# Optimization experiments

Measured on AMD Instinct MI355X. Metric: run time of the kernel, lower is better.

## Reference

```python
import jax, jax.numpy as jnp
import numpy as np

T, B, IN, HID, OUT = 100, 2048, 784, 100, 10
BETA = 0.9      # snn.Leaky(beta=0.9)
THRESH = 1.0    # snntorch default threshold
ALPHA = 2.0     # snntorch default ATan surrogate alpha

@jax.custom_vjp
def fire(x):
    # Heaviside spike with ATan surrogate gradient (snntorch default).
    return (x > 0).astype(x.dtype)

def _fire_fwd(x):
    return fire(x), x

def _fire_bwd(x, g):
    return (g * (ALPHA / 2) / (1 + (jnp.pi / 2 * ALPHA * x) ** 2),)

fire.defvjp(_fire_fwd, _fire_bwd)

def setup_inputs() -> dict:
    key = jax.random.key(0)
    k1, k2, k3 = jax.random.split(key, 3)
    x_seq = jax.random.normal(k1, (T, B, IN), dtype=jnp.float32)
    # nn.Linear weights are [out_features, in_features], bias=False
    w1 = jax.random.normal(k2, (HID, IN), dtype=jnp.float32) * (1.0 / np.sqrt(IN))
    w2 = jax.random.normal(k3, (OUT, HID), dtype=jnp.float32) * (1.0 / np.sqrt(HID))
    return {"x_seq": x_seq, "w1": w1, "w2": w2}

def _leaky_step(mem, cur):
    # snntorch Leaky, reset_mechanism='subtract':
    # reset = H(mem_prev - thresh) (detached); mem = beta*mem + input - reset*thresh; spk = fire(mem - thresh)
    reset = jax.lax.stop_gradient((mem > THRESH).astype(mem.dtype))
    mem = BETA * mem + cur - reset * THRESH
    spk = fire(mem - THRESH)
    return spk, mem

def reference(x_seq, w1, w2):
    batch = x_seq.shape[1]
    def step(carry, x_t):
        mem1, mem2 = carry
        spk1, mem1 = _leaky_step(mem1, x_t @ w1.T)      # [B,HID]
        spk2, mem2 = _leaky_step(mem2, spk1 @ w2.T)     # [B,OUT]
        return (mem1, mem2), spk2
    init = (jnp.zeros((batch, HID), x_seq.dtype),
            jnp.zeros((batch, OUT), x_seq.dtype))
    _, spk2_seq = jax.lax.scan(step, init, x_seq)
    return spk2_seq.sum(axis=0)  # spk2_sum: [B, OUT]
```

## Files before the change

kernel.cpp:

```cpp
#include <hip/hip_runtime.h>

#define T_STEPS 100
#define B_SZ    2048
#define IN_DIM  784
#define HID_DIM 100
#define OUT_DIM 10
#define BN      112
#define BMR     64
#define KC      16
#define NSTEP   (IN_DIM / KC)
#define XLP     84
#define WLP     112

typedef double f64x4 __attribute__((ext_vector_type(4)));
#define MFMA64(a, b, c) __builtin_amdgcn_mfma_f64_16x16x4f64((a), (b), (c), 0, 0, 0)

__global__ void pad_w1(const float* __restrict__ w1, float* __restrict__ w1p) {
  int i = blockIdx.x * 256 + threadIdx.x;
  if (i < BN * IN_DIM) w1p[i] = (i < HID_DIM * IN_DIM) ? w1[i] : 0.0f;
}

__global__ __launch_bounds__(256, 4)
void snn_gemm1(const float* __restrict__ x,
               const float* __restrict__ w1p,
               double* __restrict__ cur)
{
  const int tid  = threadIdx.x;
  const int lane = tid & 63;
  const int wv   = tid >> 6;
  const int kg   = lane >> 4;
  const int il   = lane & 15;
  const long rowBase = (long)blockIdx.x * BMR;

  __shared__ float xls[2][KC][XLP];
  __shared__ float wls[2][KC][WLP];

  const int xrow = tid >> 2;
  const int xq   = (tid & 3) * 4;
  const float* xsrc = x + (rowBase + xrow) * (long)IN_DIM + xq;
  const int  wrow = tid >> 1;
  const int  skh  = (tid & 1) * 8;
  const float* wsrc = w1p + (long)wrow * IN_DIM + skh;
  const bool   dow  = tid < 2 * BN;

  float4 xg, wa, wb;
  auto LOAD = [&](int s) {
    xg = *reinterpret_cast<const float4*>(xsrc + s * KC);
    if (dow) {
      const float4* wp = reinterpret_cast<const float4*>(wsrc + s * KC);
      wa = wp[0]; wb = wp[1];
    }
  };
  auto STORE = [&](int buf) {
    xls[buf][xq + 0][xrow] = xg.x; xls[buf][xq + 1][xrow] = xg.y;
    xls[buf][xq + 2][xrow] = xg.z; xls[buf][xq + 3][xrow] = xg.w;
    if (dow) {
      wls[buf][skh + 0][wrow] = wa.x; wls[buf][skh + 1][wrow] = wa.y;
      wls[buf][skh + 2][wrow] = wa.z; wls[buf][skh + 3][wrow] = wa.w;
      wls[buf][skh + 4][wrow] = wb.x; wls[buf][skh + 5][wrow] = wb.y;
      wls[buf][skh + 6][wrow] = wb.z; wls[buf][skh + 7][wrow] = wb.w;
    }
  };

  LOAD(0);

  f64x4 z = {0.0, 0.0, 0.0, 0.0};
  const double eil = (double)il;
  const double d0 = (kg == 0) ? 1.0 : 0.0;
  const double d1 = (kg == 1) ? 1.0 : 0.0;
  const double d2 = (kg == 2) ? 1.0 : 0.0;
  const double d3 = (kg == 3) ? 1.0 : 0.0;
  const f64x4 Prow0 = MFMA64(eil, d0, z);
  const f64x4 Prow1 = MFMA64(eil, d1, z);
  const f64x4 Pcol0 = MFMA64(d0, eil, z);
  const f64x4 Pcol1 = MFMA64(d1, eil, z);
  const f64x4 Pv0   = MFMA64(d0, d0, z);
  const f64x4 Pv1   = MFMA64(d1, d1, z);
  const f64x4 Pv2   = MFMA64(d2, d2, z);
  const f64x4 Pv3   = MFMA64(d3, d3, z);

  bool okl = true;
  int rowof[4], colof[4];
#pragma unroll
  for (int r = 0; r < 4; ++r) {
    okl = okl && (Pv0[r] == 1.0) && (Pv1[r] == 1.0) && (Pv2[r] == 1.0) && (Pv3[r] == 1.0);
    okl = okl && (Prow0[r] == Prow1[r]) && (Pcol0[r] == Pcol1[r]);
    const int rr = (int)Prow0[r];
    const int cc = (int)Pcol0[r];
    okl = okl && ((double)rr == Prow0[r]) && (rr >= 0) && (rr < 16);
    okl = okl && ((double)cc == Pcol0[r]) && (cc >= 0) && (cc < 16);
    rowof[r] = rr; colof[r] = cc;
  }
  if (__all(okl ? 1 : 0) == 0) {
#pragma unroll
    for (int r = 0; r < 4; ++r) { rowof[r] = kg * 4 + r; colof[r] = il; }
  }

  f64x4 acc[7];
#pragma unroll
  for (int ht = 0; ht < 7; ++ht) acc[ht] = z;

  STORE(0); LOAD(1);
  __syncthreads();

#pragma unroll 1
  for (int s = 0; s < NSTEP; ++s) {
    if (s + 1 < NSTEP) STORE((s + 1) & 1);
    if (s + 2 < NSTEP) LOAD(s + 2);
    const int buf = s & 1;

#pragma unroll
    for (int kk = 0; kk < 4; ++kk) {
      const int kr = kk * 4 + kg;
      const double a0 = (double)xls[buf][kr][wv * 16 + il];
      double b[7];
#pragma unroll
      for (int ht = 0; ht < 7; ++ht)
        b[ht] = (double)wls[buf][kr][ht * 16 + il];
#pragma unroll
      for (int ht = 0; ht < 7; ++ht)
        acc[ht] = MFMA64(a0, b[ht], acc[ht]);
    }
    __syncthreads();
  }

  const long r0 = rowBase + wv * 16;
#pragma unroll
  for (int ht = 0; ht < 7; ++ht)
#pragma unroll
    for (int m = 0; m < 4; ++m)
      cur[(r0 + rowof[m]) * BN + ht * 16 + colof[m]] = acc[ht][m];
}

__global__ __launch_bounds__(256)
void snn_recur(const double* __restrict__ cur,
               const float* __restrict__ w2,
               double* __restrict__ mem1s, float* __restrict__ spk1s,
               double* __restrict__ mem2s, float* __restrict__ spk2s,
               float* __restrict__ outs,
               float* __restrict__ dout,
               int chunkT, int isFirst, int isLast)
{
  const int tid = threadIdx.x;
  const int b0  = blockIdx.x * 4;
  __shared__ float w2l[OUT_DIM * HID_DIM];
  __shared__ float spkl[4 * BN];

  if (tid < 250)
    reinterpret_cast<float4*>(w2l)[tid] = reinterpret_cast<const float4*>(w2)[tid];

  const bool pa = tid < 112;
  const int  sl = tid / 28, q4 = (tid % 28) * 4;
  const long aOff = (long)(b0 + sl) * BN + q4;
  double m1[4] = {0.0, 0.0, 0.0, 0.0};
  float4 s1 = make_float4(0.f, 0.f, 0.f, 0.f);
  if (pa && !isFirst) {
    const double2* mp = reinterpret_cast<const double2*>(mem1s + aOff);
    double2 a = mp[0], b = mp[1];
    m1[0] = a.x; m1[1] = a.y; m1[2] = b.x; m1[3] = b.y;
    s1 = *reinterpret_cast<const float4*>(spk1s + aOff);
  }

  const bool pb = tid < 80;
  const int  pp = tid >> 1, hf = tid & 1;
  const int  ss = pp / 10, oo = pp % 10;
  const long bOff = (long)b0 * OUT_DIM + pp;
  double m2 = 0.0;
  float s2 = 0.f, oacc = 0.f;
  if (pb && !isFirst && hf == 0) { m2 = mem2s[bOff]; s2 = spk2s[bOff]; oacc = outs[bOff]; }

  __syncthreads();

  double2 ca, cb;
  if (pa) {
    const double2* cp = reinterpret_cast<const double2*>(cur + (long)b0 * BN + sl * BN + q4);
    ca = cp[0]; cb = cp[1];
  }

  for (int tt = 0; tt < chunkT; ++tt) {
    if (pa) {
      double cu[4] = {ca.x, ca.y, cb.x, cb.y};
      const int tn = (tt + 1 < chunkT) ? tt + 1 : tt;
      const double2* cp = reinterpret_cast<const double2*>(
          cur + ((long)tn * B_SZ + b0 + sl) * BN + q4);
      ca = cp[0]; cb = cp[1];

      float4 sp;
      float* spv = &sp.x;
      const float* s1v = &s1.x;
#pragma unroll
      for (int j = 0; j < 4; ++j) {
        double m = 0.9 * m1[j];
        m = m + cu[j];
        m = m - (double)s1v[j];
        spv[j] = (m > 1.0) ? 1.0f : 0.0f;
        m1[j] = m;
      }
      s1 = sp;
      *reinterpret_cast<float4*>(&spkl[sl * BN + q4]) = sp;
    }
    __syncthreads();
    if (pb) {
      const float* sr = &spkl[ss * BN] + hf * 50;
      const float* wr = &w2l[oo * HID_DIM] + hf * 50;
      double a0 = 0.0, a1 = 0.0;
#pragma unroll
      for (int h = 0; h < 50; h += 2) {
        a0 = fma((double)sr[h],     (double)wr[h],     a0);
        a1 = fma((double)sr[h + 1], (double)wr[h + 1], a1);
      }
      double a = a0 + a1;
      a = a + __shfl_xor(a, 1);
      if (hf == 0) {
        double m = 0.9 * m2;
        m = m + a;
        m = m - (double)s2;
        const float sp = (m > 1.0) ? 1.0f : 0.0f;
        m2 = m; s2 = sp; oacc += sp;
      }
    }
    __syncthreads();
  }

  if (pa) {
    double2* mp = reinterpret_cast<double2*>(mem1s + aOff);
    mp[0] = make_double2(m1[0], m1[1]);
    mp[1] = make_double2(m1[2], m1[3]);
    *reinterpret_cast<float4*>(spk1s + aOff) = s1;
  }
  if (pb && hf == 0) {
    mem2s[bOff] = m2; spk2s[bOff] = s2; outs[bOff] = oacc;
    if (isLast) dout[bOff] = oacc;
  }
}

extern "C" void kernel_launch(void* const* d_in, const int* in_sizes, int n_in,
                              void* d_out, int out_size, void* d_ws, size_t ws_size,
                              hipStream_t stream) {
  const float* x  = (const float*)d_in[0];
  const float* w1 = (const float*)d_in[1];
  const float* w2 = (const float*)d_in[2];
  float* out = (float*)d_out;

  char* ws = (char*)d_ws;
  float*  w1p   = (float*) (ws);
  double* mem1s = (double*)(ws +  351232);
  float*  spk1s = (float*) (ws + 2186240);
  double* mem2s = (double*)(ws + 3103744);
  float*  spk2s = (float*) (ws + 3267584);
  float*  outs  = (float*) (ws + 3349504);
  double* cur   = (double*)(ws + 3431424);

  pad_w1<<<dim3((BN * IN_DIM + 255) / 256), dim3(256), 0, stream>>>(w1, w1p);

  const size_t perT = (size_t)B_SZ * BN * 8;
  size_t curCap = ws_size > (size_t)3431424 ? ws_size - 3431424 : 0;
  int Tc = (int)(curCap / perT);
  if (Tc > T_STEPS) Tc = T_STEPS;
  if (Tc < 1) Tc = 1;

  for (int t0 = 0; t0 < T_STEPS; t0 += Tc) {
    const int ct = (T_STEPS - t0 < Tc) ? (T_STEPS - t0) : Tc;
    snn_gemm1<<<dim3(ct * (B_SZ / BMR)), dim3(256), 0, stream>>>(
        x + (size_t)t0 * B_SZ * IN_DIM, w1p, cur);
    snn_recur<<<dim3(B_SZ / 4), dim3(256), 0, stream>>>(
        cur, w2, mem1s, spk1s, mem2s, spk2s, outs, out,
        ct, (t0 == 0) ? 1 : 0, (t0 + ct >= T_STEPS) ? 1 : 0);
  }
}
```

Before: 724.8 us.

## Load x operands directly into registers and double the GEMM K chunk

The x tile is no longer staged through shared memory. Each lane now loads its 8 consecutive K values straight from global memory into registers and prefetches the next chunk one step ahead. The K chunk grows from 16 to 32, with w1 padded to K=800 and the tail zero-filled, which halves the number of barrier-separated loop iterations. The w1 LDS row pitch becomes 113 to reduce bank conflicts. The cost is more registers for the x prefetch and global x reads that are less coalesced across lanes.

```diff
diff --git a/kernel.cpp b/kernel.cpp
--- a/kernel.cpp
+++ b/kernel.cpp
@@ -3,21 +3,23 @@
 #define T_STEPS 100
 #define B_SZ    2048
 #define IN_DIM  784
+#define KPAD    800
 #define HID_DIM 100
 #define OUT_DIM 10
 #define BN      112
 #define BMR     64
-#define KC      16
-#define NSTEP   (IN_DIM / KC)
-#define XLP     84
-#define WLP     112
+#define KC      32
+#define KSTEPS  25
+#define WLP     113
 
 typedef double f64x4 __attribute__((ext_vector_type(4)));
 #define MFMA64(a, b, c) __builtin_amdgcn_mfma_f64_16x16x4f64((a), (b), (c), 0, 0, 0)
 
 __global__ void pad_w1(const float* __restrict__ w1, float* __restrict__ w1p) {
   int i = blockIdx.x * 256 + threadIdx.x;
-  if (i < BN * IN_DIM) w1p[i] = (i < HID_DIM * IN_DIM) ? w1[i] : 0.0f;
+  if (i >= BN * KPAD) return;
+  int r = i / KPAD, c = i % KPAD;
+  w1p[i] = (r < HID_DIM && c < IN_DIM) ? w1[r * IN_DIM + c] : 0.0f;
 }
 
 __global__ __launch_bounds__(256, 4)
@@ -32,37 +34,44 @@
   const int il   = lane & 15;
   const long rowBase = (long)blockIdx.x * BMR;
 
-  __shared__ float xls[2][KC][XLP];
   __shared__ float wls[2][KC][WLP];
 
-  const int xrow = tid >> 2;
-  const int xq   = (tid & 3) * 4;
-  const float* xsrc = x + (rowBase + xrow) * (long)IN_DIM + xq;
   const int  wrow = tid >> 1;
-  const int  skh  = (tid & 1) * 8;
-  const float* wsrc = w1p + (long)wrow * IN_DIM + skh;
-  const bool   dow  = tid < 2 * BN;
-
-  float4 xg, wa, wb;
-  auto LOAD = [&](int s) {
-    xg = *reinterpret_cast<const float4*>(xsrc + s * KC);
+  const int  wk0  = (tid & 1) * 16;
+  const bool dow  = tid < 2 * BN;
+  const float* wsrc = w1p + (long)wrow * KPAD + wk0;
+  float4 wg0, wg1, wg2, wg3;
+
+  auto WLOAD = [&](int s) {
     if (dow) {
       const float4* wp = reinterpret_cast<const float4*>(wsrc + s * KC);
-      wa = wp[0]; wb = wp[1];
+      wg0 = wp[0]; wg1 = wp[1]; wg2 = wp[2]; wg3 = wp[3];
     }
   };
-  auto STORE = [&](int buf) {
-    xls[buf][xq + 0][xrow] = xg.x; xls[buf][xq + 1][xrow] = xg.y;
-    xls[buf][xq + 2][xrow] = xg.z; xls[buf][xq + 3][xrow] = xg.w;
+  auto WSTORE = [&](int buf) {
     if (dow) {
-      wls[buf][skh + 0][wrow] = wa.x; wls[buf][skh + 1][wrow] = wa.y;
-      wls[buf][skh + 2][wrow] = wa.z; wls[buf][skh + 3][wrow] = wa.w;
-      wls[buf][skh + 4][wrow] = wb.x; wls[buf][skh + 5][wrow] = wb.y;
-      wls[buf][skh + 6][wrow] = wb.z; wls[buf][skh + 7][wrow] = wb.w;
+      float* b0 = &wls[buf][wk0][wrow];
+      b0[0 * WLP] = wg0.x; b0[1 * WLP] = wg0.y; b0[2 * WLP]  = wg0.z; b0[3 * WLP]  = wg0.w;
+      b0[4 * WLP] = wg1.x; b0[5 * WLP] = wg1.y; b0[6 * WLP]  = wg1.z; b0[7 * WLP]  = wg1.w;
+      b0[8 * WLP] = wg2.x; b0[9 * WLP] = wg2.y; b0[10 * WLP] = wg2.z; b0[11 * WLP] = wg2.w;
+      b0[12 * WLP] = wg3.x; b0[13 * WLP] = wg3.y; b0[14 * WLP] = wg3.z; b0[15 * WLP] = wg3.w;
     }
   };
 
-  LOAD(0);
+  const float* xrp = x + (rowBase + wv * 16 + il) * (long)IN_DIM;
+  float xcur[8], xnxt[8];
+  auto XLOAD = [&](int s, float* d) {
+    const int ks = s * KC + 8 * kg;
+    if (s == KSTEPS - 1 && kg >= 2) {
+#pragma unroll
+      for (int j = 0; j < 8; ++j) d[j] = 0.0f;
+    } else {
+      *reinterpret_cast<float4*>(&d[0]) = *reinterpret_cast<const float4*>(xrp + ks);
+      *reinterpret_cast<float4*>(&d[4]) = *reinterpret_cast<const float4*>(xrp + ks + 4);
+    }
+  };
+
+  WLOAD(0); XLOAD(0, xcur);
 
   f64x4 z = {0.0, 0.0, 0.0, 0.0};
   const double eil = (double)il;
@@ -100,28 +109,29 @@
 #pragma unroll
   for (int ht = 0; ht < 7; ++ht) acc[ht] = z;
 
-  STORE(0); LOAD(1);
+  WSTORE(0); WLOAD(1);
   __syncthreads();
 
 #pragma unroll 1
-  for (int s = 0; s < NSTEP; ++s) {
-    if (s + 1 < NSTEP) STORE((s + 1) & 1);
-    if (s + 2 < NSTEP) LOAD(s + 2);
+  for (int s = 0; s < KSTEPS; ++s) {
     const int buf = s & 1;
-
-#pragma unroll
-    for (int kk = 0; kk < 4; ++kk) {
-      const int kr = kk * 4 + kg;
-      const double a0 = (double)xls[buf][kr][wv * 16 + il];
+    if (s + 1 < KSTEPS) { WSTORE(buf ^ 1); XLOAD(s + 1, xnxt); }
+    if (s + 2 < KSTEPS) WLOAD(s + 2);
+
+#pragma unroll
+    for (int m = 0; m < 8; ++m) {
+      const double a0 = (double)xcur[m];
       double b[7];
 #pragma unroll
       for (int ht = 0; ht < 7; ++ht)
-        b[ht] = (double)wls[buf][kr][ht * 16 + il];
+        b[ht] = (double)wls[buf][8 * kg + m][ht * 16 + il];
 #pragma unroll
       for (int ht = 0; ht < 7; ++ht)
         acc[ht] = MFMA64(a0, b[ht], acc[ht]);
     }
     __syncthreads();
+#pragma unroll
+    for (int j = 0; j < 8; ++j) xcur[j] = xnxt[j];
   }
 
   const long r0 = rowBase + wv * 16;
@@ -173,7 +183,7 @@
 
   double2 ca, cb;
   if (pa) {
-    const double2* cp = reinterpret_cast<const double2*>(cur + (long)b0 * BN + sl * BN + q4);
+    const double2* cp = reinterpret_cast<const double2*>(cur + (long)(b0 + sl) * BN + q4);
     ca = cp[0]; cb = cp[1];
   }
 
@@ -244,17 +254,17 @@
 
   char* ws = (char*)d_ws;
   float*  w1p   = (float*) (ws);
-  double* mem1s = (double*)(ws +  351232);
-  float*  spk1s = (float*) (ws + 2186240);
-  double* mem2s = (double*)(ws + 3103744);
-  float*  spk2s = (float*) (ws + 3267584);
-  float*  outs  = (float*) (ws + 3349504);
-  double* cur   = (double*)(ws + 3431424);
-
-  pad_w1<<<dim3((BN * IN_DIM + 255) / 256), dim3(256), 0, stream>>>(w1, w1p);
+  double* mem1s = (double*)(ws +  358400);
+  float*  spk1s = (float*) (ws + 2193408);
+  double* mem2s = (double*)(ws + 3110912);
+  float*  spk2s = (float*) (ws + 3274752);
+  float*  outs  = (float*) (ws + 3356672);
+  double* cur   = (double*)(ws + 3438592);
+
+  pad_w1<<<dim3((BN * KPAD + 255) / 256), dim3(256), 0, stream>>>(w1, w1p);
 
   const size_t perT = (size_t)B_SZ * BN * 8;
-  size_t curCap = ws_size > (size_t)3431424 ? ws_size - 3431424 : 0;
+  size_t curCap = ws_size > (size_t)3438592 ? ws_size - 3438592 : 0;
   int Tc = (int)(curCap / perT);
   if (Tc > T_STEPS) Tc = T_STEPS;
   if (Tc < 1) Tc = 1;
```

Result: slower. 771.5 us (+6.5%).

## Drop hidden-dim padding and process two timesteps per barrier in recurrence

Applied to the files above, without the earlier changes.

The hidden dimension is no longer padded from 100 to 112. The GEMM computes 6 FP64 MFMA tiles, adds the last 4 columns with scalar FMAs plus a cross-lane reduction, and reads w1 directly, so the pad kernel is gone. The intermediate current buffer uses a stride of 100, which cuts its size and global traffic. The recurrence kernel now advances two timesteps between each pair of barriers, using a double-buffered spike tile in shared memory, to halve the synchronisation count. The price is extra scalar FMA work in the GEMM inner loop and more register pressure.

```diff
diff --git a/kernel.cpp b/kernel.cpp
--- a/kernel.cpp
+++ b/kernel.cpp
@@ -5,7 +5,7 @@
 #define IN_DIM  784
 #define HID_DIM 100
 #define OUT_DIM 10
-#define BN      112
+#define CSTR    100
 #define BMR     64
 #define KC      16
 #define NSTEP   (IN_DIM / KC)
@@ -15,14 +15,9 @@
 typedef double f64x4 __attribute__((ext_vector_type(4)));
 #define MFMA64(a, b, c) __builtin_amdgcn_mfma_f64_16x16x4f64((a), (b), (c), 0, 0, 0)
 
-__global__ void pad_w1(const float* __restrict__ w1, float* __restrict__ w1p) {
-  int i = blockIdx.x * 256 + threadIdx.x;
-  if (i < BN * IN_DIM) w1p[i] = (i < HID_DIM * IN_DIM) ? w1[i] : 0.0f;
-}
-
 __global__ __launch_bounds__(256, 4)
 void snn_gemm1(const float* __restrict__ x,
-               const float* __restrict__ w1p,
+               const float* __restrict__ w1,
                double* __restrict__ cur)
 {
   const int tid  = threadIdx.x;
@@ -40,8 +35,8 @@
   const float* xsrc = x + (rowBase + xrow) * (long)IN_DIM + xq;
   const int  wrow = tid >> 1;
   const int  skh  = (tid & 1) * 8;
-  const float* wsrc = w1p + (long)wrow * IN_DIM + skh;
-  const bool   dow  = tid < 2 * BN;
+  const float* wsrc = w1 + (long)wrow * IN_DIM + skh;
+  const bool   dow  = tid < 2 * HID_DIM;
 
   float4 xg, wa, wb;
   auto LOAD = [&](int s) {
@@ -96,9 +91,10 @@
     for (int r = 0; r < 4; ++r) { rowof[r] = kg * 4 + r; colof[r] = il; }
   }
 
-  f64x4 acc[7];
-#pragma unroll
-  for (int ht = 0; ht < 7; ++ht) acc[ht] = z;
+  f64x4 acc[6];
+#pragma unroll
+  for (int ht = 0; ht < 6; ++ht) acc[ht] = z;
+  double acc4[4] = {0.0, 0.0, 0.0, 0.0};
 
   STORE(0); LOAD(1);
   __syncthreads();
@@ -113,23 +109,38 @@
     for (int kk = 0; kk < 4; ++kk) {
       const int kr = kk * 4 + kg;
       const double a0 = (double)xls[buf][kr][wv * 16 + il];
-      double b[7];
-#pragma unroll
-      for (int ht = 0; ht < 7; ++ht)
+      double b[6];
+#pragma unroll
+      for (int ht = 0; ht < 6; ++ht)
         b[ht] = (double)wls[buf][kr][ht * 16 + il];
 #pragma unroll
-      for (int ht = 0; ht < 7; ++ht)
+      for (int ht = 0; ht < 6; ++ht)
         acc[ht] = MFMA64(a0, b[ht], acc[ht]);
+      const float4 wt = *reinterpret_cast<const float4*>(&wls[buf][kr][96]);
+      acc4[0] = fma(a0, (double)wt.x, acc4[0]);
+      acc4[1] = fma(a0, (double)wt.y, acc4[1]);
+      acc4[2] = fma(a0, (double)wt.z, acc4[2]);
+      acc4[3] = fma(a0, (double)wt.w, acc4[3]);
     }
     __syncthreads();
   }
 
+#pragma unroll
+  for (int c = 0; c < 4; ++c) {
+    acc4[c] += __shfl_xor(acc4[c], 16);
+    acc4[c] += __shfl_xor(acc4[c], 32);
+  }
+
   const long r0 = rowBase + wv * 16;
 #pragma unroll
-  for (int ht = 0; ht < 7; ++ht)
+  for (int ht = 0; ht < 6; ++ht)
 #pragma unroll
     for (int m = 0; m < 4; ++m)
-      cur[(r0 + rowof[m]) * BN + ht * 16 + colof[m]] = acc[ht][m];
+      cur[(r0 + rowof[m]) * CSTR + ht * 16 + colof[m]] = acc[ht][m];
+  if (kg == 0) {
+    double* cp = cur + (r0 + il) * CSTR + 96;
+    cp[0] = acc4[0]; cp[1] = acc4[1]; cp[2] = acc4[2]; cp[3] = acc4[3];
+  }
 }
 
 __global__ __launch_bounds__(256)
@@ -144,14 +155,14 @@
   const int tid = threadIdx.x;
   const int b0  = blockIdx.x * 4;
   __shared__ float w2l[OUT_DIM * HID_DIM];
-  __shared__ float spkl[4 * BN];
+  __shared__ float spkl[2][4 * HID_DIM];
 
   if (tid < 250)
     reinterpret_cast<float4*>(w2l)[tid] = reinterpret_cast<const float4*>(w2)[tid];
 
-  const bool pa = tid < 112;
-  const int  sl = tid / 28, q4 = (tid % 28) * 4;
-  const long aOff = (long)(b0 + sl) * BN + q4;
+  const bool pa = tid < 100;
+  const int  sl = tid / 25, q4 = (tid % 25) * 4;
+  const long aOff = (long)(b0 + sl) * HID_DIM + q4;
   double m1[4] = {0.0, 0.0, 0.0, 0.0};
   float4 s1 = make_float4(0.f, 0.f, 0.f, 0.f);
   if (pa && !isFirst) {
@@ -171,52 +182,80 @@
 
   __syncthreads();
 
-  double2 ca, cb;
+  double2 ca0, cb0, ca1, cb1;
   if (pa) {
-    const double2* cp = reinterpret_cast<const double2*>(cur + (long)b0 * BN + sl * BN + q4);
-    ca = cp[0]; cb = cp[1];
-  }
-
-  for (int tt = 0; tt < chunkT; ++tt) {
+    const double2* cp0 = reinterpret_cast<const double2*>(cur + aOff);
+    ca0 = cp0[0]; cb0 = cp0[1];
+    const int t1 = (chunkT > 1) ? 1 : 0;
+    const double2* cp1 = reinterpret_cast<const double2*>(
+        cur + (long)t1 * B_SZ * HID_DIM + aOff);
+    ca1 = cp1[0]; cb1 = cp1[1];
+  }
+
+  for (int tt = 0; tt < chunkT; tt += 2) {
+    const bool two = (tt + 1 < chunkT);
     if (pa) {
-      double cu[4] = {ca.x, ca.y, cb.x, cb.y};
-      const int tn = (tt + 1 < chunkT) ? tt + 1 : tt;
-      const double2* cp = reinterpret_cast<const double2*>(
-          cur + ((long)tn * B_SZ + b0 + sl) * BN + q4);
-      ca = cp[0]; cb = cp[1];
-
-      float4 sp;
-      float* spv = &sp.x;
+      double cu0[4] = {ca0.x, ca0.y, cb0.x, cb0.y};
+      double cu1[4] = {ca1.x, ca1.y, cb1.x, cb1.y};
+      const int tn2 = (tt + 2 < chunkT) ? tt + 2 : chunkT - 1;
+      const int tn3 = (tt + 3 < chunkT) ? tt + 3 : chunkT - 1;
+      const double2* cp2 = reinterpret_cast<const double2*>(
+          cur + (long)tn2 * B_SZ * HID_DIM + aOff);
+      ca0 = cp2[0]; cb0 = cp2[1];
+      const double2* cp3 = reinterpret_cast<const double2*>(
+          cur + (long)tn3 * B_SZ * HID_DIM + aOff);
+      ca1 = cp3[0]; cb1 = cp3[1];
+
+      float4 sp0, sp1;
+      float* sp0v = &sp0.x; float* sp1v = &sp1.x;
       const float* s1v = &s1.x;
 #pragma unroll
       for (int j = 0; j < 4; ++j) {
         double m = 0.9 * m1[j];
-        m = m + cu[j];
+        m = m + cu0[j];
         m = m - (double)s1v[j];
-        spv[j] = (m > 1.0) ? 1.0f : 0.0f;
+        sp0v[j] = (m > 1.0) ? 1.0f : 0.0f;
         m1[j] = m;
       }
-      s1 = sp;
-      *reinterpret_cast<float4*>(&spkl[sl * BN + q4]) = sp;
+      if (two) {
+#pragma unroll
+        for (int j = 0; j < 4; ++j) {
+          double m = 0.9 * m1[j];
+          m = m + cu1[j];
+          m = m - (double)sp0v[j];
+          sp1v[j] = (m > 1.0) ? 1.0f : 0.0f;
+          m1[j] = m;
+        }
+        s1 = sp1;
+      } else {
+        s1 = sp0;
+      }
+      *reinterpret_cast<float4*>(&spkl[0][sl * HID_DIM + q4]) = sp0;
+      if (two)
+        *reinterpret_cast<float4*>(&spkl[1][sl * HID_DIM + q4]) = sp1;
     }
     __syncthreads();
     if (pb) {
-      const float* sr = &spkl[ss * BN] + hf * 50;
       const float* wr = &w2l[oo * HID_DIM] + hf * 50;
-      double a0 = 0.0, a1 = 0.0;
-#pragma unroll
-      for (int h = 0; h < 50; h += 2) {
-        a0 = fma((double)sr[h],     (double)wr[h],     a0);
-        a1 = fma((double)sr[h + 1], (double)wr[h + 1], a1);
-      }
-      double a = a0 + a1;
-      a = a + __shfl_xor(a, 1);
-      if (hf == 0) {
-        double m = 0.9 * m2;
-        m = m + a;
-        m = m - (double)s2;
-        const float sp = (m > 1.0) ? 1.0f : 0.0f;
-        m2 = m; s2 = sp; oacc += sp;
+#pragma unroll 1
+      for (int u = 0; u < 2; ++u) {
+        if (u == 1 && !two) break;
+        const float* sr = &spkl[u][ss * HID_DIM] + hf * 50;
+        double a0 = 0.0, a1 = 0.0;
+#pragma unroll
+        for (int h = 0; h < 50; h += 2) {
+          a0 = fma((double)sr[h],     (double)wr[h],     a0);
+          a1 = fma((double)sr[h + 1], (double)wr[h + 1], a1);
+        }
+        double a = a0 + a1;
+        a = a + __shfl_xor(a, 1);
+        if (hf == 0) {
+          double m = 0.9 * m2;
+          m = m + a;
+          m = m - (double)s2;
+          const float sp = (m > 1.0) ? 1.0f : 0.0f;
+          m2 = m; s2 = sp; oacc += sp;
+        }
       }
     }
     __syncthreads();
@@ -243,18 +282,15 @@
   float* out = (float*)d_out;
 
   char* ws = (char*)d_ws;
-  float*  w1p   = (float*) (ws);
-  double* mem1s = (double*)(ws +  351232);
-  float*  spk1s = (float*) (ws + 2186240);
-  double* mem2s = (double*)(ws + 3103744);
-  float*  spk2s = (float*) (ws + 3267584);
-  float*  outs  = (float*) (ws + 3349504);
-  double* cur   = (double*)(ws + 3431424);
-
-  pad_w1<<<dim3((BN * IN_DIM + 255) / 256), dim3(256), 0, stream>>>(w1, w1p);
-
-  const size_t perT = (size_t)B_SZ * BN * 8;
-  size_t curCap = ws_size > (size_t)3431424 ? ws_size - 3431424 : 0;
+  double* mem1s = (double*)(ws);
+  float*  spk1s = (float*) (ws + 1638400);
+  double* mem2s = (double*)(ws + 2457600);
+  float*  spk2s = (float*) (ws + 2621440);
+  float*  outs  = (float*) (ws + 2703360);
+  double* cur   = (double*)(ws + 2785280);
+
+  const size_t perT = (size_t)B_SZ * HID_DIM * 8;
+  size_t curCap = ws_size > (size_t)2785280 ? ws_size - 2785280 : 0;
   int Tc = (int)(curCap / perT);
   if (Tc > T_STEPS) Tc = T_STEPS;
   if (Tc < 1) Tc = 1;
@@ -262,7 +298,7 @@
   for (int t0 = 0; t0 < T_STEPS; t0 += Tc) {
     const int ct = (T_STEPS - t0 < Tc) ? (T_STEPS - t0) : Tc;
     snn_gemm1<<<dim3(ct * (B_SZ / BMR)), dim3(256), 0, stream>>>(
-        x + (size_t)t0 * B_SZ * IN_DIM, w1p, cur);
+        x + (size_t)t0 * B_SZ * IN_DIM, w1, cur);
     snn_recur<<<dim3(B_SZ / 4), dim3(256), 0, stream>>>(
         cur, w2, mem1s, spk1s, mem2s, spk2s, outs, out,
         ct, (t0 == 0) ? 1 : 0, (t0 + ct >= T_STEPS) ? 1 : 0);
```

Result: faster. 675.8 us, median of 2 (-6.8%).
